# Kernel tuning notes

Measured on AMD Instinct MI355X. Metric: run time of the kernel, lower is better.

## Reference

```python
import jax, jax.numpy as jnp
import numpy as np

B, N, C, HEADS = 8, 1024, 768, 12
HW = 32  # H = W = 32, so H*W == N


def _layernorm(x, g, b, eps=1e-5):
    mu = x.mean(-1, keepdims=True)
    var = ((x - mu) ** 2).mean(-1, keepdims=True)
    return (x - mu) * jax.lax.rsqrt(var + eps) * g + b


def setup_inputs() -> dict:
    key = jax.random.key(0)
    ks = jax.random.split(key, 6)
    w = lambda k, shape: jax.random.normal(k, shape, dtype=jnp.float32) * 0.02
    return {
        "x": jax.random.normal(ks[0], (B, N, C), dtype=jnp.float32),
        "y": jax.random.normal(ks[1], (B, C, HW, HW), dtype=jnp.float32),
        "q_w": w(ks[2], (C, C)),
        "q_b": jnp.zeros((C,), jnp.float32),
        "kv_w": w(ks[3], (2 * C, C)),
        "kv_b": jnp.zeros((2 * C,), jnp.float32),
        "proj_w": w(ks[4], (C, C)),
        "proj_b": jnp.zeros((C,), jnp.float32),
        "ln_g": jnp.ones((C,), jnp.float32),
        "ln_b": jnp.zeros((C,), jnp.float32),
        "H": HW,
        "W": HW,
    }


def reference(x, y, q_w, q_b, kv_w, kv_b, proj_w, proj_b, ln_g, ln_b, H, W):
    Bn, Nn, Cn = x.shape
    hd = Cn // HEADS
    scale = hd ** -0.5  # qk_scale=None, c_ratio=1 -> head_dim**-0.5

    # gating tensors from y
    y1 = y.reshape(Bn, Cn, H * W).transpose(0, 2, 1)          # [B, N, C]
    y2 = _layernorm(y1, ln_g, ln_b)
    yq = jax.nn.sigmoid(y2 @ q_w.T + q_b)                      # [B, N, C]
    ykv = jax.nn.sigmoid(y2 @ kv_w.T + kv_b)                   # [B, N, 2C]

    # gated q: q2 = q0 + q0*yq
    q0 = x @ q_w.T + q_b
    q = (q0 + q0 * yq).reshape(Bn, Nn, HEADS, hd).transpose(0, 2, 1, 3)  # [B,h,N,d]

    # gated kv: kv2 = kv0*ykv + ykv
    kv0 = x @ kv_w.T + kv_b
    kv = (kv0 * ykv + ykv).reshape(Bn, Nn, 2, HEADS, hd).transpose(2, 0, 3, 1, 4)
    k, v = kv[0], kv[1]                                        # [B,h,N,d] each

    attn = jax.nn.softmax(jnp.einsum("bhqd,bhkd->bhqk", q, k) * scale, axis=-1)
    out = jnp.einsum("bhqk,bhkd->bhqd", attn, v)
    out = out.transpose(0, 2, 1, 3).reshape(Bn, Nn, Cn)
    return out @ proj_w.T + proj_b
```

## Files before the change

### kernel.cpp

```cpp
#include <hip/hip_runtime.h>
#include <stdint.h>

typedef __attribute__((ext_vector_type(4))) float f4;
typedef __attribute__((ext_vector_type(8))) short bf16x8;
typedef __attribute__((ext_vector_type(4))) unsigned short u16x4;
typedef unsigned short u16;

#define B_ 8
#define N_ 1024
#define C_ 768
#define NH 12
#define HD 64

__device__ __forceinline__ float bf2f(u16 v) {
  union { unsigned u; float f; } x; x.u = ((unsigned)v) << 16; return x.f;
}
__device__ __forceinline__ u16 f2bf(float f) {
  union { float f; unsigned u; } x; x.f = f;
  unsigned r = x.u + 0x7FFFu + ((x.u >> 16) & 1u);
  return (u16)(r >> 16);
}
__device__ __forceinline__ void g2l16(const u16* g, const u16* l) {
  __builtin_amdgcn_global_load_lds(
      (const __attribute__((address_space(1))) void*)(uintptr_t)g,
      (__attribute__((address_space(3))) void*)(uint32_t)(uintptr_t)l,
      16, 0, 0);
}

__global__ __launch_bounds__(256) void cvt_bf16(const float* __restrict__ s,
                                                u16* __restrict__ d, int n4) {
  int i = blockIdx.x * 256 + threadIdx.x;
  int stride = gridDim.x * 256;
  for (; i < n4; i += stride) {
    float4 v = ((const float4*)s)[i];
    u16x4 o;
    o.x = f2bf(v.x); o.y = f2bf(v.y); o.z = f2bf(v.z); o.w = f2bf(v.w);
    ((u16x4*)d)[i] = o;
  }
}

__global__ __launch_bounds__(256) void ln_stats(const float* __restrict__ y,
                                                float* __restrict__ mu,
                                                float* __restrict__ rs,
                                                int b0) {
  __shared__ float s1[4][64], s2[4][64];
  int t = threadIdx.x;
  int nl = t & 63, ch = t >> 6;
  int idx0 = b0 * N_ + blockIdx.x * 64;
  int b = idx0 >> 10, nb_ = idx0 & 1023;
  const float* p = y + (size_t)b * C_ * N_ + nb_ + nl;
  float s = 0.f, q = 0.f;
  int c0 = ch * 192;
  for (int c = c0; c < c0 + 192; ++c) {
    float v = p[(size_t)c * N_];
    s += v; q += v * v;
  }
  s1[ch][nl] = s; s2[ch][nl] = q;
  __syncthreads();
  if (t < 64) {
    float ts = s1[0][t] + s1[1][t] + s1[2][t] + s1[3][t];
    float tq = s2[0][t] + s2[1][t] + s2[2][t] + s2[3][t];
    float m = ts * (1.f / C_);
    float var = tq * (1.f / C_) - m * m;
    mu[idx0 + t] = m;
    rs[idx0 + t] = rsqrtf(fmaxf(var, 0.f) + 1e-5f);
  }
}

__global__ __launch_bounds__(256) void ln_apply(const float* __restrict__ y,
                                                const float* __restrict__ mu,
                                                const float* __restrict__ rs,
                                                const float* __restrict__ lg,
                                                const float* __restrict__ lb,
                                                u16* __restrict__ y2c,
                                                int b0) {
  __shared__ float tile[64][65];
  int t = threadIdx.x;
  int n0 = blockIdx.x * 64, c0 = blockIdx.y * 64;
  int bl = blockIdx.z, b = b0 + bl;
  int jc = (t & 15) * 4, ir = t >> 4;
  for (int r = 0; r < 4; ++r) {
    int i = ir + r * 16;
    float4 v = *(const float4*)(y + ((size_t)b * C_ + c0 + i) * N_ + n0 + jc);
    tile[i][jc] = v.x; tile[i][jc + 1] = v.y; tile[i][jc + 2] = v.z; tile[i][jc + 3] = v.w;
  }
  __syncthreads();
  for (int r = 0; r < 4; ++r) {
    int i = ir + r * 16;
    int n = n0 + i;
    float m = mu[b * N_ + n], rr = rs[b * N_ + n];
    float g0 = lg[c0 + jc],     b0f = lb[c0 + jc];
    float g1 = lg[c0 + jc + 1], b1f = lb[c0 + jc + 1];
    float g2 = lg[c0 + jc + 2], b2f = lb[c0 + jc + 2];
    float g3 = lg[c0 + jc + 3], b3f = lb[c0 + jc + 3];
    u16x4 o;
    o.x = f2bf((tile[jc][i] - m) * rr * g0 + b0f);
    o.y = f2bf((tile[jc + 1][i] - m) * rr * g1 + b1f);
    o.z = f2bf((tile[jc + 2][i] - m) * rr * g2 + b2f);
    o.w = f2bf((tile[jc + 3][i] - m) * rr * g3 + b3f);
    *(u16x4*)(y2c + ((size_t)bl * N_ + n) * C_ + c0 + jc) = o;
  }
}

__global__ __launch_bounds__(256, 2) void gemm_gate(
    const u16* __restrict__ xbc, const u16* __restrict__ y2c,
    const u16* __restrict__ qwb, const u16* __restrict__ kvwb,
    const float* __restrict__ qb_, const float* __restrict__ kvb_,
    u16* __restrict__ o_q, u16* __restrict__ o_k, u16* __restrict__ o_vT) {
  __shared__ u16 smem[24576];
  int t = threadIdx.x, l = t & 63;
  int quad = l >> 4, l15 = l & 15;
  int w = t >> 6, wm = w & 1, wn = w >> 1;
  int m0l = blockIdx.x * 128;
  int n0l = blockIdx.y * 128;

  const u16* wp; const float* bp; int sel, h0;
  if (n0l < C_) {
    wp = qwb + (size_t)n0l * C_; bp = qb_ + n0l; sel = 0; h0 = n0l >> 6;
  } else {
    int nk = n0l - C_;
    wp = kvwb + (size_t)nk * C_; bp = kvb_ + nk;
    sel = (nk < C_) ? 1 : 2;
    h0 = ((sel == 2) ? nk - C_ : nk) >> 6;
  }

  f4 accx[4][4], accy[4][4];
  for (int i = 0; i < 4; ++i)
    for (int j = 0; j < 4; ++j) {
      accx[i][j] = (f4){0.f, 0.f, 0.f, 0.f};
      accy[i][j] = (f4){0.f, 0.f, 0.f, 0.f};
    }

  int row = t >> 2, colb = (t & 3) * 8;
  const u16* gx = xbc + (size_t)(m0l + row) * C_ + colb;
  const u16* gy = y2c + (size_t)(m0l + row) * C_ + colb;
  const u16* gw = wp + (size_t)row * C_ + colb;

#define STAGE_G(bb, kk)                                        \
  do {                                                         \
    u16* Axp = smem + (bb) * 12288;                            \
    g2l16(gx + (kk),           Axp + t * 8);                   \
    g2l16(gx + (kk) + 64 * C_, Axp + 2048 + t * 8);            \
    g2l16(gy + (kk),           Axp + 4096 + t * 8);            \
    g2l16(gy + (kk) + 64 * C_, Axp + 6144 + t * 8);            \
    g2l16(gw + (kk),           Axp + 8192 + t * 8);            \
    g2l16(gw + (kk) + 64 * C_, Axp + 10240 + t * 8);           \
  } while (0)

  STAGE_G(0, 0);
  __syncthreads();
  for (int s = 0; s < 24; ++s) {
    if (s < 23) STAGE_G((s + 1) & 1, (s + 1) * 32);
    const u16* base = smem + (s & 1) * 12288;
    bf16x8 afx[4], afy[4], bfr[4];
    for (int i = 0; i < 4; ++i) {
      int ra = (wm * 64 + i * 16 + l15) * 32 + quad * 8;
      afx[i] = *(const bf16x8*)&base[ra];
      afy[i] = *(const bf16x8*)&base[4096 + ra];
      int rb = (wn * 64 + i * 16 + l15) * 32 + quad * 8;
      bfr[i] = *(const bf16x8*)&base[8192 + rb];
    }
    for (int i = 0; i < 4; ++i)
      for (int j = 0; j < 4; ++j) {
        accx[i][j] = __builtin_amdgcn_mfma_f32_16x16x32_bf16(afx[i], bfr[j], accx[i][j], 0, 0, 0);
        accy[i][j] = __builtin_amdgcn_mfma_f32_16x16x32_bf16(afy[i], bfr[j], accy[i][j], 0, 0, 0);
      }
    __syncthreads();
  }
#undef STAGE_G

  const int PITCH = 136;
  for (int j = 0; j < 4; ++j) {
    int cloc = wn * 64 + j * 16 + l15;
    float bias = bp[cloc];
    for (int i = 0; i < 4; ++i) {
      int rb0 = wm * 64 + i * 16 + quad * 4;
      for (int r = 0; r < 4; ++r) {
        int rloc = rb0 + r;
        float vx = accx[i][j][r] + bias;
        float vy = accy[i][j][r] + bias;
        float gg = 1.f / (1.f + __expf(-vy));
        float val = (sel == 0) ? vx * (1.f + gg) : gg * (vx + 1.f);
        u16 bv = f2bf(val);
        if (sel == 2) smem[cloc * PITCH + rloc] = bv;
        else          smem[rloc * PITCH + cloc] = bv;
      }
    }
  }
  __syncthreads();
  {
    int rr = t >> 1, hh = t & 1;
    const u16* src = smem + rr * PITCH + hh * 64;
    u16* dst;
    if (sel == 2) {
      int h = h0 + (rr >> 6), d = rr & 63;
      int bl = m0l >> 10, nbase = m0l & 1023;
      dst = o_vT + (size_t)((bl * NH + h) * HD + d) * N_ + nbase + hh * 64;
    } else {
      int gml = m0l + rr;
      int bl = gml >> 10, n = gml & 1023;
      int h = h0 + hh;
      dst = (sel == 0 ? o_q : o_k) + (size_t)((bl * NH + h) * N_ + n) * HD;
    }
    for (int c = 0; c < 8; ++c) {
      bf16x8 v = *(const bf16x8*)(src + c * 8);
      *(bf16x8*)(dst + c * 8) = v;
    }
  }
}

__global__ __launch_bounds__(256) void attn(const u16* __restrict__ qoc,
                                            const u16* __restrict__ koc,
                                            const u16* __restrict__ vTc,
                                            u16* __restrict__ aoc) {
  __shared__ u16 Qs[4096], Ks[2][4096], Vs[2][4096];
  __shared__ u16 Ps[64 * 72];
  int t = threadIdx.x, l = t & 63, w = t >> 6;
  int quad = l >> 4, l15 = l & 15;
  int bhl = blockIdx.y;
  int bl = bhl / NH, h = bhl % NH;
  int q0 = blockIdx.x * 64;
  int sr = t >> 3;
  int swo = ((t & 7) ^ (sr & 7)) * 8;
  const u16* qbp = qoc + ((size_t)bhl * N_ + q0) * HD;
  const u16* kb = koc + (size_t)bhl * N_ * HD;
  const u16* vb = vTc + (size_t)bhl * HD * N_;

  g2l16(qbp + sr * HD + swo,        Qs + t * 8);
  g2l16(qbp + (32 + sr) * HD + swo, Qs + 2048 + t * 8);

#define STAGE_KV(bb, key0)                                          \
  do {                                                              \
    g2l16(kb + (size_t)((key0) + sr) * HD + swo,      Ks[bb] + t * 8);        \
    g2l16(kb + (size_t)((key0) + 32 + sr) * HD + swo, Ks[bb] + 2048 + t * 8); \
    g2l16(vb + (size_t)sr * N_ + (key0) + swo,        Vs[bb] + t * 8);        \
    g2l16(vb + (size_t)(32 + sr) * N_ + (key0) + swo, Vs[bb] + 2048 + t * 8); \
  } while (0)

  STAGE_KV(0, 0);
  __syncthreads();

  int sA = (quad ^ (l15 & 7)) * 8;
  int sB = sA ^ 32;
  bf16x8 aq0 = *(const bf16x8*)&Qs[(w * 16 + l15) * 64 + sA];
  bf16x8 aq1 = *(const bf16x8*)&Qs[(w * 16 + l15) * 64 + sB];
  f4 o[4];
  for (int i = 0; i < 4; ++i) o[i] = (f4){0.f, 0.f, 0.f, 0.f};
  float lsum[4] = {0.f, 0.f, 0.f, 0.f};

  for (int kt = 0; kt < 16; ++kt) {
    int cur = kt & 1;
    if (kt < 15) STAGE_KV(cur ^ 1, (kt + 1) * 64);
    f4 s[4];
    __builtin_amdgcn_s_setprio(1);
    for (int ni = 0; ni < 4; ++ni) {
      bf16x8 b0v = *(const bf16x8*)&Ks[cur][(ni * 16 + l15) * 64 + sA];
      bf16x8 b1v = *(const bf16x8*)&Ks[cur][(ni * 16 + l15) * 64 + sB];
      f4 z = (f4){0.f, 0.f, 0.f, 0.f};
      z = __builtin_amdgcn_mfma_f32_16x16x32_bf16(aq0, b0v, z, 0, 0, 0);
      z = __builtin_amdgcn_mfma_f32_16x16x32_bf16(aq1, b1v, z, 0, 0, 0);
      s[ni] = z;
    }
    __builtin_amdgcn_s_setprio(0);
    float p[4][4];
    for (int ni = 0; ni < 4; ++ni)
      for (int r = 0; r < 4; ++r)
        p[ni][r] = __expf(s[ni][r] * 0.125f);
    for (int r = 0; r < 4; ++r) {
      float ts = p[0][r] + p[1][r] + p[2][r] + p[3][r];
      ts += __shfl_xor(ts, 1);
      ts += __shfl_xor(ts, 2);
      ts += __shfl_xor(ts, 4);
      ts += __shfl_xor(ts, 8);
      lsum[r] += ts;
    }
    for (int ni = 0; ni < 4; ++ni)
      for (int r = 0; r < 4; ++r)
        Ps[(w * 16 + quad * 4 + r) * 72 + ni * 16 + l15] = f2bf(p[ni][r]);
    bf16x8 ap0 = *(const bf16x8*)&Ps[(w * 16 + l15) * 72 + quad * 8];
    bf16x8 ap1 = *(const bf16x8*)&Ps[(w * 16 + l15) * 72 + 32 + quad * 8];
    __builtin_amdgcn_s_setprio(1);
    for (int ni = 0; ni < 4; ++ni) {
      bf16x8 b0v = *(const bf16x8*)&Vs[cur][(ni * 16 + l15) * 64 + sA];
      bf16x8 b1v = *(const bf16x8*)&Vs[cur][(ni * 16 + l15) * 64 + sB];
      o[ni] = __builtin_amdgcn_mfma_f32_16x16x32_bf16(ap0, b0v, o[ni], 0, 0, 0);
      o[ni] = __builtin_amdgcn_mfma_f32_16x16x32_bf16(ap1, b1v, o[ni], 0, 0, 0);
    }
    __builtin_amdgcn_s_setprio(0);
    __syncthreads();
  }
#undef STAGE_KV

  for (int ni = 0; ni < 4; ++ni)
    for (int r = 0; r < 4; ++r)
      Ps[(w * 16 + quad * 4 + r) * 72 + ni * 16 + l15] =
          f2bf(o[ni][r] / lsum[r]);
  __syncthreads();
  {
    int rr = t >> 2, cc = t & 3;
    int n = q0 + rr;
    const u16* src = Ps + rr * 72 + cc * 16;
    u16* dst = aoc + ((size_t)bl * N_ + n) * C_ + h * HD + cc * 16;
    *(bf16x8*)dst = *(const bf16x8*)src;
    *(bf16x8*)(dst + 8) = *(const bf16x8*)(src + 8);
  }
}

__global__ __launch_bounds__(256, 2) void gemm_proj(const u16* __restrict__ aoc,
                                                    const u16* __restrict__ pwb,
                                                    const float* __restrict__ bias,
                                                    float* __restrict__ out,
                                                    int b0) {
  __shared__ u16 smem[16384];
  int t = threadIdx.x, l = t & 63;
  int quad = l >> 4, l15 = l & 15;
  int w = t >> 6, wm = w & 1, wn = w >> 1;
  int m0l = blockIdx.x * 128, n0 = blockIdx.y * 128;
  f4 acc[4][4];
  for (int i = 0; i < 4; ++i)
    for (int j = 0; j < 4; ++j) acc[i][j] = (f4){0.f, 0.f, 0.f, 0.f};
  int row = t >> 2, colb = (t & 3) * 8;
  const u16* ga = aoc + (size_t)(m0l + row) * C_ + colb;
  const u16* gw = pwb + (size_t)(n0 + row) * C_ + colb;

#define STAGE_P(bb, kk)                                        \
  do {                                                         \
    u16* Asp = smem + (bb) * 8192;                             \
    g2l16(ga + (kk),           Asp + t * 8);                   \
    g2l16(ga + (kk) + 64 * C_, Asp + 2048 + t * 8);            \
    g2l16(gw + (kk),           Asp + 4096 + t * 8);            \
    g2l16(gw + (kk) + 64 * C_, Asp + 6144 + t * 8);            \
  } while (0)

  STAGE_P(0, 0);
  __syncthreads();
  for (int s = 0; s < 24; ++s) {
    if (s < 23) STAGE_P((s + 1) & 1, (s + 1) * 32);
    const u16* base = smem + (s & 1) * 8192;
    bf16x8 af[4], bfr[4];
    for (int i = 0; i < 4; ++i) {
      af[i]  = *(const bf16x8*)&base[(wm * 64 + i * 16 + l15) * 32 + quad * 8];
      bfr[i] = *(const bf16x8*)&base[4096 + (wn * 64 + i * 16 + l15) * 32 + quad * 8];
    }
    for (int i = 0; i < 4; ++i)
      for (int j = 0; j < 4; ++j)
        acc[i][j] = __builtin_amdgcn_mfma_f32_16x16x32_bf16(af[i], bfr[j], acc[i][j], 0, 0, 0);
    __syncthreads();
  }
#undef STAGE_P

  for (int j = 0; j < 4; ++j) {
    int gcol = n0 + wn * 64 + j * 16 + l15;
    float bv = bias[gcol];
    for (int i = 0; i < 4; ++i) {
      int rbase = m0l + wm * 64 + i * 16 + quad * 4;
      for (int r = 0; r < 4; ++r)
        __builtin_nontemporal_store(acc[i][j][r] + bv,
                                    &out[(size_t)(b0 * N_ + rbase + r) * C_ + gcol]);
    }
  }
}

extern "C" void kernel_launch(void* const* d_in, const int* in_sizes, int n_in,
                              void* d_out, int out_size, void* d_ws, size_t ws_size,
                              hipStream_t stream) {
  const float* x   = (const float*)d_in[0];
  const float* y   = (const float*)d_in[1];
  const float* qw  = (const float*)d_in[2];
  const float* qb  = (const float*)d_in[3];
  const float* kvw = (const float*)d_in[4];
  const float* kvb = (const float*)d_in[5];
  const float* pw  = (const float*)d_in[6];
  const float* pb  = (const float*)d_in[7];
  const float* lg  = (const float*)d_in[8];
  const float* lb  = (const float*)d_in[9];

  char* ws = (char*)d_ws;
  float* mu = (float*)(ws);
  float* rs = (float*)(ws + 32768);
  u16* qwb  = (u16*)(ws + 65536);
  u16* kvwb = (u16*)(ws + 1245184);
  u16* pwb  = (u16*)(ws + 3604480);
  const size_t BASE2 = 4784128;
  const size_t PER_B = 1572864;

  int nb = 1;
  for (int c = 8; c >= 1; c >>= 1) {
    if (BASE2 + 5 * (size_t)c * PER_B <= ws_size) { nb = c; break; }
  }
  u16* xbc = (u16*)(ws + BASE2);
  u16* y2c = (u16*)(ws + BASE2 + (size_t)nb * PER_B);
  u16* qoc = (u16*)(ws + BASE2 + 2 * (size_t)nb * PER_B);
  u16* koc = (u16*)(ws + BASE2 + 3 * (size_t)nb * PER_B);
  u16* vTc = (u16*)(ws + BASE2 + 4 * (size_t)nb * PER_B);
  u16* aoc = xbc;

  cvt_bf16<<<dim3(576), dim3(256), 0, stream>>>(qw, qwb, 147456);
  cvt_bf16<<<dim3(1152), dim3(256), 0, stream>>>(kvw, kvwb, 294912);
  cvt_bf16<<<dim3(576), dim3(256), 0, stream>>>(pw, pwb, 147456);

  for (int b0 = 0; b0 < B_; b0 += nb) {
    cvt_bf16<<<dim3(768 * nb), dim3(256), 0, stream>>>(
        x + (size_t)b0 * N_ * C_, xbc, nb * 196608);
    ln_stats<<<dim3(16 * nb), dim3(256), 0, stream>>>(y, mu, rs, b0);
    ln_apply<<<dim3(16, 12, nb), dim3(256), 0, stream>>>(y, mu, rs, lg, lb, y2c, b0);
    gemm_gate<<<dim3(8 * nb, 18), dim3(256), 0, stream>>>(xbc, y2c, qwb, kvwb,
                                                          qb, kvb, qoc, koc, vTc);
    attn<<<dim3(16, 12 * nb), dim3(256), 0, stream>>>(qoc, koc, vTc, aoc);
    gemm_proj<<<dim3(8 * nb, 6), dim3(256), 0, stream>>>(aoc, pwb, pb, (float*)d_out, b0);
  }
}
```

Baseline: 304.9 us.

## Use explicit vmcnt waits and barriers, MFMA row sums, narrower proj tiles

Replaces __syncthreads-based double buffering in gemm_gate, attn and gemm_proj with manually unrolled ping-pong stages. Each stage uses explicit s_waitcnt vmcnt counts and raw barriers, so the next tile's global-to-LDS loads stay in flight while the current tile computes. In attention, the softmax denominator is now accumulated by an MFMA against a ones vector instead of shuffle reductions. gemm_proj tiles drop from 128x128 to 128x64 to double the grid. The hand-written waitcnt counts rely on exact load ordering and could break if the compiler reorders or adds memory ops.

New measurement: 281.5 us. 1.08x faster.

```diff
diff --git a/kernel.cpp b/kernel.cpp
--- a/kernel.cpp
+++ b/kernel.cpp
@@ -26,6 +26,17 @@
       (__attribute__((address_space(3))) void*)(uint32_t)(uintptr_t)l,
       16, 0, 0);
 }
+
+#define SW6() asm volatile("s_waitcnt vmcnt(6)" ::: "memory")
+#define SW4() asm volatile("s_waitcnt vmcnt(4)" ::: "memory")
+#define SW3() asm volatile("s_waitcnt vmcnt(3)" ::: "memory")
+#define SW0() asm volatile("s_waitcnt vmcnt(0)" ::: "memory")
+#define BARF()                              \
+  do {                                      \
+    __builtin_amdgcn_s_barrier();           \
+    asm volatile("" ::: "memory");          \
+    __builtin_amdgcn_sched_barrier(0);      \
+  } while (0)
 
 __global__ __launch_bounds__(256) void cvt_bf16(const float* __restrict__ s,
                                                 u16* __restrict__ d, int n4) {
@@ -136,38 +147,51 @@
   const u16* gy = y2c + (size_t)(m0l + row) * C_ + colb;
   const u16* gw = wp + (size_t)row * C_ + colb;
 
-#define STAGE_G(bb, kk)                                        \
-  do {                                                         \
-    u16* Axp = smem + (bb) * 12288;                            \
-    g2l16(gx + (kk),           Axp + t * 8);                   \
-    g2l16(gx + (kk) + 64 * C_, Axp + 2048 + t * 8);            \
-    g2l16(gy + (kk),           Axp + 4096 + t * 8);            \
-    g2l16(gy + (kk) + 64 * C_, Axp + 6144 + t * 8);            \
-    g2l16(gw + (kk),           Axp + 8192 + t * 8);            \
-    g2l16(gw + (kk) + 64 * C_, Axp + 10240 + t * 8);           \
+#define STAGE_G(OFF, kk)                                   \
+  do {                                                     \
+    u16* p_ = smem + (OFF);                                \
+    g2l16(gx + (kk),           p_ + t * 8);                \
+    g2l16(gx + (kk) + 64 * C_, p_ + 2048 + t * 8);         \
+    g2l16(gy + (kk),           p_ + 4096 + t * 8);         \
+    g2l16(gy + (kk) + 64 * C_, p_ + 6144 + t * 8);         \
+    g2l16(gw + (kk),           p_ + 8192 + t * 8);         \
+    g2l16(gw + (kk) + 64 * C_, p_ + 10240 + t * 8);        \
+  } while (0)
+
+#define COMPUTE_G(OFF)                                                        \
+  do {                                                                        \
+    const u16* base = smem + (OFF);                                           \
+    bf16x8 afx[4], afy[4], bfr[4];                                            \
+    for (int i = 0; i < 4; ++i) {                                             \
+      int ra = (wm * 64 + i * 16 + l15) * 32 + quad * 8;                      \
+      afx[i] = *(const bf16x8*)&base[ra];                                     \
+      afy[i] = *(const bf16x8*)&base[4096 + ra];                              \
+      int rb = (wn * 64 + i * 16 + l15) * 32 + quad * 8;                      \
+      bfr[i] = *(const bf16x8*)&base[8192 + rb];                              \
+    }                                                                         \
+    for (int i = 0; i < 4; ++i)                                               \
+      for (int j = 0; j < 4; ++j) {                                           \
+        accx[i][j] = __builtin_amdgcn_mfma_f32_16x16x32_bf16(afx[i], bfr[j], accx[i][j], 0, 0, 0); \
+        accy[i][j] = __builtin_amdgcn_mfma_f32_16x16x32_bf16(afy[i], bfr[j], accy[i][j], 0, 0, 0); \
+      }                                                                       \
   } while (0)
 
   STAGE_G(0, 0);
-  __syncthreads();
-  for (int s = 0; s < 24; ++s) {
-    if (s < 23) STAGE_G((s + 1) & 1, (s + 1) * 32);
-    const u16* base = smem + (s & 1) * 12288;
-    bf16x8 afx[4], afy[4], bfr[4];
-    for (int i = 0; i < 4; ++i) {
-      int ra = (wm * 64 + i * 16 + l15) * 32 + quad * 8;
-      afx[i] = *(const bf16x8*)&base[ra];
-      afy[i] = *(const bf16x8*)&base[4096 + ra];
-      int rb = (wn * 64 + i * 16 + l15) * 32 + quad * 8;
-      bfr[i] = *(const bf16x8*)&base[8192 + rb];
-    }
-    for (int i = 0; i < 4; ++i)
-      for (int j = 0; j < 4; ++j) {
-        accx[i][j] = __builtin_amdgcn_mfma_f32_16x16x32_bf16(afx[i], bfr[j], accx[i][j], 0, 0, 0);
-        accy[i][j] = __builtin_amdgcn_mfma_f32_16x16x32_bf16(afy[i], bfr[j], accy[i][j], 0, 0, 0);
-      }
-    __syncthreads();
+  STAGE_G(12288, 32);
+  SW6();
+  BARF();
+  for (int n = 0; n < 24; n += 2) {
+    COMPUTE_G(0);
+    BARF();
+    if (n + 2 < 24) { STAGE_G(0, (n + 2) * 32); SW6(); } else { SW0(); }
+    BARF();
+    COMPUTE_G(12288);
+    BARF();
+    if (n + 3 < 24) { STAGE_G(12288, (n + 3) * 32); SW6(); } else { SW0(); }
+    BARF();
   }
 #undef STAGE_G
+#undef COMPUTE_G
 
   const int PITCH = 136;
   for (int j = 0; j < 4; ++j) {
@@ -213,7 +237,7 @@
                                             const u16* __restrict__ koc,
                                             const u16* __restrict__ vTc,
                                             u16* __restrict__ aoc) {
-  __shared__ u16 Qs[4096], Ks[2][4096], Vs[2][4096];
+  __shared__ u16 Qs[4096], Ks[8192], Vs[8192];
   __shared__ u16 Ps[64 * 72];
   int t = threadIdx.x, l = t & 63, w = t >> 6;
   int quad = l >> 4, l15 = l & 15;
@@ -226,19 +250,20 @@
   const u16* kb = koc + (size_t)bhl * N_ * HD;
   const u16* vb = vTc + (size_t)bhl * HD * N_;
 
+#define STAGE_KV(OFF, key0)                                                   \
+  do {                                                                        \
+    g2l16(kb + (size_t)((key0) + sr) * HD + swo,      Ks + (OFF) + t * 8);    \
+    g2l16(kb + (size_t)((key0) + 32 + sr) * HD + swo, Ks + (OFF) + 2048 + t * 8); \
+    g2l16(vb + (size_t)sr * N_ + (key0) + swo,        Vs + (OFF) + t * 8);    \
+    g2l16(vb + (size_t)(32 + sr) * N_ + (key0) + swo, Vs + (OFF) + 2048 + t * 8); \
+  } while (0)
+
   g2l16(qbp + sr * HD + swo,        Qs + t * 8);
   g2l16(qbp + (32 + sr) * HD + swo, Qs + 2048 + t * 8);
-
-#define STAGE_KV(bb, key0)                                          \
-  do {                                                              \
-    g2l16(kb + (size_t)((key0) + sr) * HD + swo,      Ks[bb] + t * 8);        \
-    g2l16(kb + (size_t)((key0) + 32 + sr) * HD + swo, Ks[bb] + 2048 + t * 8); \
-    g2l16(vb + (size_t)sr * N_ + (key0) + swo,        Vs[bb] + t * 8);        \
-    g2l16(vb + (size_t)(32 + sr) * N_ + (key0) + swo, Vs[bb] + 2048 + t * 8); \
-  } while (0)
-
   STAGE_KV(0, 0);
-  __syncthreads();
+  STAGE_KV(4096, 64);
+  SW4();
+  BARF();
 
   int sA = (quad ^ (l15 & 7)) * 8;
   int sB = sA ^ 32;
@@ -246,55 +271,58 @@
   bf16x8 aq1 = *(const bf16x8*)&Qs[(w * 16 + l15) * 64 + sB];
   f4 o[4];
   for (int i = 0; i < 4; ++i) o[i] = (f4){0.f, 0.f, 0.f, 0.f};
-  float lsum[4] = {0.f, 0.f, 0.f, 0.f};
-
-  for (int kt = 0; kt < 16; ++kt) {
-    int cur = kt & 1;
-    if (kt < 15) STAGE_KV(cur ^ 1, (kt + 1) * 64);
-    f4 s[4];
-    __builtin_amdgcn_s_setprio(1);
-    for (int ni = 0; ni < 4; ++ni) {
-      bf16x8 b0v = *(const bf16x8*)&Ks[cur][(ni * 16 + l15) * 64 + sA];
-      bf16x8 b1v = *(const bf16x8*)&Ks[cur][(ni * 16 + l15) * 64 + sB];
-      f4 z = (f4){0.f, 0.f, 0.f, 0.f};
-      z = __builtin_amdgcn_mfma_f32_16x16x32_bf16(aq0, b0v, z, 0, 0, 0);
-      z = __builtin_amdgcn_mfma_f32_16x16x32_bf16(aq1, b1v, z, 0, 0, 0);
-      s[ni] = z;
-    }
-    __builtin_amdgcn_s_setprio(0);
-    float p[4][4];
-    for (int ni = 0; ni < 4; ++ni)
-      for (int r = 0; r < 4; ++r)
-        p[ni][r] = __expf(s[ni][r] * 0.125f);
-    for (int r = 0; r < 4; ++r) {
-      float ts = p[0][r] + p[1][r] + p[2][r] + p[3][r];
-      ts += __shfl_xor(ts, 1);
-      ts += __shfl_xor(ts, 2);
-      ts += __shfl_xor(ts, 4);
-      ts += __shfl_xor(ts, 8);
-      lsum[r] += ts;
-    }
-    for (int ni = 0; ni < 4; ++ni)
-      for (int r = 0; r < 4; ++r)
-        Ps[(w * 16 + quad * 4 + r) * 72 + ni * 16 + l15] = f2bf(p[ni][r]);
-    bf16x8 ap0 = *(const bf16x8*)&Ps[(w * 16 + l15) * 72 + quad * 8];
-    bf16x8 ap1 = *(const bf16x8*)&Ps[(w * 16 + l15) * 72 + 32 + quad * 8];
-    __builtin_amdgcn_s_setprio(1);
-    for (int ni = 0; ni < 4; ++ni) {
-      bf16x8 b0v = *(const bf16x8*)&Vs[cur][(ni * 16 + l15) * 64 + sA];
-      bf16x8 b1v = *(const bf16x8*)&Vs[cur][(ni * 16 + l15) * 64 + sB];
-      o[ni] = __builtin_amdgcn_mfma_f32_16x16x32_bf16(ap0, b0v, o[ni], 0, 0, 0);
-      o[ni] = __builtin_amdgcn_mfma_f32_16x16x32_bf16(ap1, b1v, o[ni], 0, 0, 0);
-    }
-    __builtin_amdgcn_s_setprio(0);
-    __syncthreads();
-  }
+  f4 ls = (f4){0.f, 0.f, 0.f, 0.f};
+  bf16x8 ones;
+  for (int i = 0; i < 8; ++i) ones[i] = (short)0x3F80;
+
+#define TILE_STEP(KOFF)                                                       \
+  do {                                                                        \
+    f4 s_[4];                                                                 \
+    __builtin_amdgcn_s_setprio(1);                                            \
+    for (int ni = 0; ni < 4; ++ni) {                                          \
+      bf16x8 b0v = *(const bf16x8*)&Ks[(KOFF) + (ni * 16 + l15) * 64 + sA];   \
+      bf16x8 b1v = *(const bf16x8*)&Ks[(KOFF) + (ni * 16 + l15) * 64 + sB];   \
+      f4 z = (f4){0.f, 0.f, 0.f, 0.f};                                        \
+      z = __builtin_amdgcn_mfma_f32_16x16x32_bf16(aq0, b0v, z, 0, 0, 0);      \
+      z = __builtin_amdgcn_mfma_f32_16x16x32_bf16(aq1, b1v, z, 0, 0, 0);      \
+      s_[ni] = z;                                                             \
+    }                                                                         \
+    __builtin_amdgcn_s_setprio(0);                                            \
+    for (int ni = 0; ni < 4; ++ni)                                            \
+      for (int r = 0; r < 4; ++r)                                             \
+        Ps[(w * 16 + quad * 4 + r) * 72 + ni * 16 + l15] =                    \
+            f2bf(__expf(s_[ni][r] * 0.125f));                                 \
+    bf16x8 ap0 = *(const bf16x8*)&Ps[(w * 16 + l15) * 72 + quad * 8];         \
+    bf16x8 ap1 = *(const bf16x8*)&Ps[(w * 16 + l15) * 72 + 32 + quad * 8];    \
+    __builtin_amdgcn_s_setprio(1);                                            \
+    for (int ni = 0; ni < 4; ++ni) {                                          \
+      bf16x8 b0v = *(const bf16x8*)&Vs[(KOFF) + (ni * 16 + l15) * 64 + sA];   \
+      bf16x8 b1v = *(const bf16x8*)&Vs[(KOFF) + (ni * 16 + l15) * 64 + sB];   \
+      o[ni] = __builtin_amdgcn_mfma_f32_16x16x32_bf16(ap0, b0v, o[ni], 0, 0, 0); \
+      o[ni] = __builtin_amdgcn_mfma_f32_16x16x32_bf16(ap1, b1v, o[ni], 0, 0, 0); \
+    }                                                                         \
+    ls = __builtin_amdgcn_mfma_f32_16x16x32_bf16(ap0, ones, ls, 0, 0, 0);     \
+    ls = __builtin_amdgcn_mfma_f32_16x16x32_bf16(ap1, ones, ls, 0, 0, 0);     \
+    __builtin_amdgcn_s_setprio(0);                                            \
+  } while (0)
+
+  for (int kt = 0; kt < 16; kt += 2) {
+    TILE_STEP(0);
+    BARF();
+    if (kt + 2 < 16) { STAGE_KV(0, (kt + 2) * 64); SW4(); } else { SW0(); }
+    BARF();
+    TILE_STEP(4096);
+    BARF();
+    if (kt + 3 < 16) { STAGE_KV(4096, (kt + 3) * 64); SW4(); } else { SW0(); }
+    BARF();
+  }
+#undef TILE_STEP
 #undef STAGE_KV
 
   for (int ni = 0; ni < 4; ++ni)
     for (int r = 0; r < 4; ++r)
       Ps[(w * 16 + quad * 4 + r) * 72 + ni * 16 + l15] =
-          f2bf(o[ni][r] / lsum[r]);
+          f2bf(o[ni][r] / ls[r]);
   __syncthreads();
   {
     int rr = t >> 2, cc = t & 3;
@@ -311,46 +339,58 @@
                                                     const float* __restrict__ bias,
                                                     float* __restrict__ out,
                                                     int b0) {
-  __shared__ u16 smem[16384];
+  __shared__ u16 smem[12288];
   int t = threadIdx.x, l = t & 63;
   int quad = l >> 4, l15 = l & 15;
   int w = t >> 6, wm = w & 1, wn = w >> 1;
-  int m0l = blockIdx.x * 128, n0 = blockIdx.y * 128;
-  f4 acc[4][4];
+  int m0l = blockIdx.x * 128, n0 = blockIdx.y * 64;
+  f4 acc[4][2];
   for (int i = 0; i < 4; ++i)
-    for (int j = 0; j < 4; ++j) acc[i][j] = (f4){0.f, 0.f, 0.f, 0.f};
+    for (int j = 0; j < 2; ++j) acc[i][j] = (f4){0.f, 0.f, 0.f, 0.f};
   int row = t >> 2, colb = (t & 3) * 8;
   const u16* ga = aoc + (size_t)(m0l + row) * C_ + colb;
   const u16* gw = pwb + (size_t)(n0 + row) * C_ + colb;
 
-#define STAGE_P(bb, kk)                                        \
-  do {                                                         \
-    u16* Asp = smem + (bb) * 8192;                             \
-    g2l16(ga + (kk),           Asp + t * 8);                   \
-    g2l16(ga + (kk) + 64 * C_, Asp + 2048 + t * 8);            \
-    g2l16(gw + (kk),           Asp + 4096 + t * 8);            \
-    g2l16(gw + (kk) + 64 * C_, Asp + 6144 + t * 8);            \
+#define STAGE_P(OFF, kk)                                   \
+  do {                                                     \
+    u16* p_ = smem + (OFF);                                \
+    g2l16(ga + (kk),           p_ + t * 8);                \
+    g2l16(ga + (kk) + 64 * C_, p_ + 2048 + t * 8);         \
+    g2l16(gw + (kk),           p_ + 4096 + t * 8);         \
+  } while (0)
+
+#define COMPUTE_P(OFF)                                                        \
+  do {                                                                        \
+    const u16* base = smem + (OFF);                                           \
+    bf16x8 af[4], bfr[2];                                                     \
+    for (int i = 0; i < 4; ++i)                                               \
+      af[i] = *(const bf16x8*)&base[(wm * 64 + i * 16 + l15) * 32 + quad * 8];\
+    for (int j = 0; j < 2; ++j)                                               \
+      bfr[j] = *(const bf16x8*)&base[4096 + (wn * 32 + j * 16 + l15) * 32 + quad * 8]; \
+    for (int i = 0; i < 4; ++i)                                               \
+      for (int j = 0; j < 2; ++j)                                             \
+        acc[i][j] = __builtin_amdgcn_mfma_f32_16x16x32_bf16(af[i], bfr[j], acc[i][j], 0, 0, 0); \
   } while (0)
 
   STAGE_P(0, 0);
-  __syncthreads();
-  for (int s = 0; s < 24; ++s) {
-    if (s < 23) STAGE_P((s + 1) & 1, (s + 1) * 32);
-    const u16* base = smem + (s & 1) * 8192;
-    bf16x8 af[4], bfr[4];
-    for (int i = 0; i < 4; ++i) {
-      af[i]  = *(const bf16x8*)&base[(wm * 64 + i * 16 + l15) * 32 + quad * 8];
-      bfr[i] = *(const bf16x8*)&base[4096 + (wn * 64 + i * 16 + l15) * 32 + quad * 8];
-    }
-    for (int i = 0; i < 4; ++i)
-      for (int j = 0; j < 4; ++j)
-        acc[i][j] = __builtin_amdgcn_mfma_f32_16x16x32_bf16(af[i], bfr[j], acc[i][j], 0, 0, 0);
-    __syncthreads();
+  STAGE_P(6144, 32);
+  SW3();
+  BARF();
+  for (int n = 0; n < 24; n += 2) {
+    COMPUTE_P(0);
+    BARF();
+    if (n + 2 < 24) { STAGE_P(0, (n + 2) * 32); SW3(); } else { SW0(); }
+    BARF();
+    COMPUTE_P(6144);
+    BARF();
+    if (n + 3 < 24) { STAGE_P(6144, (n + 3) * 32); SW3(); } else { SW0(); }
+    BARF();
   }
 #undef STAGE_P
-
-  for (int j = 0; j < 4; ++j) {
-    int gcol = n0 + wn * 64 + j * 16 + l15;
+#undef COMPUTE_P
+
+  for (int j = 0; j < 2; ++j) {
+    int gcol = n0 + wn * 32 + j * 16 + l15;
     float bv = bias[gcol];
     for (int i = 0; i < 4; ++i) {
       int rbase = m0l + wm * 64 + i * 16 + quad * 4;
@@ -407,6 +447,6 @@
     gemm_gate<<<dim3(8 * nb, 18), dim3(256), 0, stream>>>(xbc, y2c, qwb, kvwb,
                                                           qb, kvb, qoc, koc, vTc);
     attn<<<dim3(16, 12 * nb), dim3(256), 0, stream>>>(qoc, koc, vTc, aoc);
-    gemm_proj<<<dim3(8 * nb, 6), dim3(256), 0, stream>>>(aoc, pwb, pb, (float*)d_out, b0);
-  }
-}
+    gemm_proj<<<dim3(8 * nb, 12), dim3(256), 0, stream>>>(aoc, pwb, pb, (float*)d_out, b0);
+  }
+}
```
